# Kernel optimization log

Measured on AMD Instinct MI355X. Metric: run time of the kernel, lower is better.

## Reference

```python
import jax, jax.numpy as jnp
import numpy as np

EMBED_DIM = 512
NUM_HEADS = 8
HEAD_DIM = EMBED_DIM // NUM_HEADS


def setup_inputs() -> dict:
    key = jax.random.key(0)
    ks = jax.random.split(key, 9)
    C = EMBED_DIM
    s = 1.0 / np.sqrt(C)
    x = jax.random.normal(ks[0], (1, 4096, C), dtype=jnp.float32)
    Wq = jax.random.uniform(ks[1], (C, C), jnp.float32, -s, s)
    bq = jax.random.uniform(ks[2], (C,), jnp.float32, -s, s)
    Wk = jax.random.uniform(ks[3], (C, C), jnp.float32, -s, s)
    bk = jax.random.uniform(ks[4], (C,), jnp.float32, -s, s)
    Wv = jax.random.uniform(ks[5], (C, C), jnp.float32, -s, s)
    bv = jax.random.uniform(ks[6], (C,), jnp.float32, -s, s)
    Wo = jax.random.uniform(ks[7], (C, C), jnp.float32, -s, s)
    bo = jax.random.uniform(ks[8], (C,), jnp.float32, -s, s)
    return {"x": x, "Wq": Wq, "bq": bq, "Wk": Wk, "bk": bk,
            "Wv": Wv, "bv": bv, "Wo": Wo, "bo": bo}


def reference(x, Wq, bq, Wk, bk, Wv, bv, Wo, bo):
    B, N, C = x.shape
    H, D = NUM_HEADS, HEAD_DIM
    # QKV projections, split into heads: [B, H, N, D]
    def proj(W, b):
        y = x @ W + b
        return y.reshape(B, N, H, D).transpose(0, 2, 1, 3)
    Q, K, V = proj(Wq, bq), proj(Wk, bk), proj(Wv, bv)
    # NOTE: original scales by 1/sqrt(embed_dim), NOT 1/sqrt(head_dim)
    scale = 1.0 / jnp.sqrt(jnp.float32(C)).astype(x.dtype)
    scores = jnp.einsum('bhnd,bhmd->bhnm', Q, K) * scale  # [B,H,N,N]
    attn = jax.nn.softmax(scores, axis=-1)
    out = jnp.einsum('bhnm,bhmd->bhnd', attn, V)  # [B,H,N,D]
    out = out.transpose(0, 2, 1, 3).reshape(B, N, C)
    return out @ Wo + bo
```

## Files before the change

kernel.cpp:

```cpp
#include <hip/hip_runtime.h>
#include <hip/hip_bf16.h>

#define SEQ 4096
#define CDIM 512
#define NHEAD 8
#define HDIM 64
#define KVB 64
#define NSPLIT 4
#define TILES_PER_SPLIT (SEQ / KVB / NSPLIT)

typedef __attribute__((ext_vector_type(8))) short bf16x8;
typedef __attribute__((ext_vector_type(4))) float f32x4;
typedef __attribute__((ext_vector_type(16))) float f32x16;

__device__ __forceinline__ short f2b(float f) {
  union { float f; unsigned u; } v; v.f = f;
  unsigned u = v.u;
  unsigned r = u + 0x7fffu + ((u >> 16) & 1u);
  return (short)(r >> 16);
}
__device__ __forceinline__ float b2f(short s) {
  union { unsigned u; float f; } v; v.u = ((unsigned)(unsigned short)s) << 16;
  return v.f;
}
__device__ __forceinline__ unsigned pk2(float a, float b) {
  union { __hip_bfloat162 h; unsigned u; } z;
  z.h = __float22bfloat162_rn(make_float2(a, b));
  return z.u;
}

__global__ __launch_bounds__(256) void prep_kernel(
    const float* __restrict__ x,
    const float* __restrict__ Wq, const float* __restrict__ Wk,
    const float* __restrict__ Wv, const float* __restrict__ Wo,
    short* __restrict__ xb,
    short* __restrict__ Wqt, short* __restrict__ Wkt,
    short* __restrict__ Wvt, short* __restrict__ Wot) {
  __shared__ short tile[32][33];
  int b = blockIdx.x, tid = threadIdx.x;
  if (b < 2048) {
    int i = (b * 256 + tid) * 4;
    float4 v = *(const float4*)(x + i);
    short4 o;
    o.x = f2b(v.x); o.y = f2b(v.y); o.z = f2b(v.z); o.w = f2b(v.w);
    *(short4*)(xb + i) = o;
    return;
  }
  int t = b - 2048;
  int mat = t >> 8; t &= 255;
  const float* W = mat == 0 ? Wq : mat == 1 ? Wk : mat == 2 ? Wv : Wo;
  short* Wt = mat == 0 ? Wqt : mat == 1 ? Wkt : mat == 2 ? Wvt : Wot;
  int n0 = (t & 15) * 32, k0 = (t >> 4) * 32;
  int tx = tid & 31, ty = tid >> 5;
  for (int i = 0; i < 32; i += 8)
    tile[ty + i][tx] = f2b(W[(size_t)(k0 + ty + i) * CDIM + n0 + tx]);
  __syncthreads();
  for (int i = 0; i < 32; i += 8)
    Wt[(size_t)(n0 + ty + i) * CDIM + k0 + tx] = tile[tx][ty + i];
}

__global__ __launch_bounds__(256) void qkv_gemm_kernel(
    const short* __restrict__ A,
    const short* __restrict__ Wqt, const short* __restrict__ Wkt, const short* __restrict__ Wvt,
    const float* __restrict__ bq, const float* __restrict__ bk, const float* __restrict__ bv,
    short* __restrict__ Qb, short* __restrict__ Kb, short* __restrict__ Vtb) {
  __shared__ short As[64 * 64];
  __shared__ short Bs[64 * 64];
  const int z = blockIdx.z;
  const short* Bt = z == 0 ? Wqt : z == 1 ? Wkt : Wvt;
  const float* bias = z == 0 ? bq : z == 1 ? bk : bv;
  const int m0 = blockIdx.x * 64, n0 = blockIdx.y * 64;
  const int tid = threadIdx.x;
  const int w = tid >> 6, lane = tid & 63, g = lane >> 4, l16 = lane & 15;
  f32x4 acc[4] = {};
  for (int kt = 0; kt < CDIM; kt += 64) {
    __syncthreads();
    for (int it = 0; it < 2; ++it) {
      int c = tid + it * 256;
      int r = c >> 3, cc = (c & 7) * 8;
      int sw = r * 64 + (cc ^ ((r & 7) * 8));
      *(bf16x8*)(As + sw) = *(const bf16x8*)(A + (size_t)(m0 + r) * CDIM + kt + cc);
      *(bf16x8*)(Bs + sw) = *(const bf16x8*)(Bt + (size_t)(n0 + r) * CDIM + kt + cc);
    }
    __syncthreads();
    const int ar = w * 16 + l16;
    for (int ks = 0; ks < 2; ++ks) {
      int c0 = ks * 32 + 8 * g;
      bf16x8 af = *(const bf16x8*)(As + ar * 64 + (c0 ^ ((ar & 7) * 8)));
      for (int ni = 0; ni < 4; ++ni) {
        int br = ni * 16 + l16;
        bf16x8 bf = *(const bf16x8*)(Bs + br * 64 + (c0 ^ ((br & 7) * 8)));
        acc[ni] = __builtin_amdgcn_mfma_f32_16x16x32_bf16(af, bf, acc[ni], 0, 0, 0);
      }
    }
  }
  for (int ni = 0; ni < 4; ++ni) {
    int col = n0 + ni * 16 + l16;
    float bv_ = bias[col];
    for (int j = 0; j < 4; ++j) {
      int row = m0 + w * 16 + g * 4 + j;
      float v = acc[ni][j] + bv_;
      if (z == 0)      Qb[(size_t)row * CDIM + col] = f2b(v);
      else if (z == 1) Kb[(size_t)row * CDIM + col] = f2b(v);
      else             Vtb[(size_t)col * SEQ + row] = f2b(v);
    }
  }
}

__global__ __launch_bounds__(256) void out_gemm_kernel(
    const short* __restrict__ A, const short* __restrict__ Bt,
    const float* __restrict__ bias, float* __restrict__ out) {
  __shared__ short As[64 * 64];
  __shared__ short Bs[64 * 64];
  const int m0 = blockIdx.x * 64, n0 = blockIdx.y * 64;
  const int tid = threadIdx.x;
  const int w = tid >> 6, lane = tid & 63, g = lane >> 4, l16 = lane & 15;
  f32x4 acc[4] = {};
  for (int kt = 0; kt < CDIM; kt += 64) {
    __syncthreads();
    for (int it = 0; it < 2; ++it) {
      int c = tid + it * 256;
      int r = c >> 3, cc = (c & 7) * 8;
      int sw = r * 64 + (cc ^ ((r & 7) * 8));
      *(bf16x8*)(As + sw) = *(const bf16x8*)(A + (size_t)(m0 + r) * CDIM + kt + cc);
      *(bf16x8*)(Bs + sw) = *(const bf16x8*)(Bt + (size_t)(n0 + r) * CDIM + kt + cc);
    }
    __syncthreads();
    const int ar = w * 16 + l16;
    for (int ks = 0; ks < 2; ++ks) {
      int c0 = ks * 32 + 8 * g;
      bf16x8 af = *(const bf16x8*)(As + ar * 64 + (c0 ^ ((ar & 7) * 8)));
      for (int ni = 0; ni < 4; ++ni) {
        int br = ni * 16 + l16;
        bf16x8 bf = *(const bf16x8*)(Bs + br * 64 + (c0 ^ ((br & 7) * 8)));
        acc[ni] = __builtin_amdgcn_mfma_f32_16x16x32_bf16(af, bf, acc[ni], 0, 0, 0);
      }
    }
  }
  for (int ni = 0; ni < 4; ++ni) {
    int col = n0 + ni * 16 + l16;
    float bv_ = bias[col];
    for (int j = 0; j < 4; ++j) {
      int row = m0 + w * 16 + g * 4 + j;
      out[(size_t)row * CDIM + col] = acc[ni][j] + bv_;
    }
  }
}

__global__ __launch_bounds__(512, 4) void attn_kernel(
    const short* __restrict__ Qb,
    const short* __restrict__ Kb,
    const short* __restrict__ Vtb,
    short* __restrict__ Op0, short* __restrict__ Op1,
    short* __restrict__ Op2, short* __restrict__ Op3,
    float* __restrict__ lpart) {
  __shared__ __align__(16) char arena[49152];
  __shared__ float lzp[4][32];
  short* KsB = (short*)arena;
  short* VsB = (short*)(arena + 24576);
  const int bid = blockIdx.x;
  const int h = bid & 7;
  const int rest = bid >> 3;
  const int split = rest & 3;
  const int q0 = (rest >> 2) * 128;
  const int kvbase = split * (TILES_PER_SPLIT * KVB);
  const int tid = threadIdx.x;
  const int wid = tid >> 6, lane = tid & 63;
  const int l31 = lane & 31, hi = lane >> 5;
  const int rh = wid >> 1, kq = wid & 1;
  const float scale2 = 0.06375872274f;

  short* Opart = split == 0 ? Op0 : split == 1 ? Op1 : split == 2 ? Op2 : Op3;

  bf16x8 qf[4];
  {
    int qrow = q0 + rh * 32 + l31;
#pragma unroll
    for (int kst = 0; kst < 4; ++kst) {
      bf16x8 q = *(const bf16x8*)(Qb + (size_t)qrow * CDIM + h * 64 + kst * 16 + hi * 8);
#pragma unroll
      for (int i = 0; i < 8; ++i) q[i] = f2b(b2f(q[i]) * scale2);
      qf[kst] = q;
    }
  }

  const int srow = tid >> 3;
  const int scol8 = 8 * ((tid & 7) ^ (srow & 7));
  const short* kstage = Kb + (size_t)(kvbase + srow) * CDIM + h * 64 + scol8;
  const short* vstage = Vtb + (size_t)(h * 64 + srow) * SEQ + kvbase + scol8;
  auto stage = [&](short* sK, short* sV) {
    __builtin_amdgcn_global_load_lds(
        (const __attribute__((address_space(1))) void*)kstage,
        (__attribute__((address_space(3))) void*)(sK + tid * 8), 16, 0, 0);
    __builtin_amdgcn_global_load_lds(
        (const __attribute__((address_space(1))) void*)vstage,
        (__attribute__((address_space(3))) void*)(sV + tid * 8), 16, 0, 0);
    kstage += KVB * CDIM;
    vstage += KVB;
  };

  f32x16 osum[2] = {};
  float lsum = 0.f;
  unsigned w[8];

  auto softmax = [&](f32x16& s) {
    float ls0 = 0.f, ls1 = 0.f;
#pragma unroll
    for (int m = 0; m < 8; ++m) {
      float p0 = __builtin_amdgcn_exp2f(s[2 * m]);
      float p1 = __builtin_amdgcn_exp2f(s[2 * m + 1]);
      ls0 += p0; ls1 += p1;
      w[m] = pk2(p0, p1);
    }
    lsum += ls0 + ls1;
  };

  auto phase = [&](const short* vbuf, const short* kbuf, short* sK, short* sV, bool do_st) {
    if (do_st) stage(sK, sV);
    union { unsigned u[4]; bf16x8 v; } pf0, pf1;
#if __has_builtin(__builtin_amdgcn_permlane32_swap)
    {
      auto a0 = __builtin_amdgcn_permlane32_swap(w[0], w[2], false, false);
      auto a1 = __builtin_amdgcn_permlane32_swap(w[1], w[3], false, false);
      auto a2 = __builtin_amdgcn_permlane32_swap(w[4], w[6], false, false);
      auto a3 = __builtin_amdgcn_permlane32_swap(w[5], w[7], false, false);
      pf0.u[0] = a0[0]; pf0.u[1] = a1[0]; pf0.u[2] = a0[1]; pf0.u[3] = a1[1];
      pf1.u[0] = a2[0]; pf1.u[1] = a3[0]; pf1.u[2] = a2[1]; pf1.u[3] = a3[1];
    }
#else
    {
      unsigned t0 = hi ? w[0] : w[2], t1 = hi ? w[1] : w[3];
      unsigned t2 = hi ? w[4] : w[6], t3 = hi ? w[5] : w[7];
      unsigned r0 = __shfl_xor(t0, 32), r1 = __shfl_xor(t1, 32);
      unsigned r2 = __shfl_xor(t2, 32), r3 = __shfl_xor(t3, 32);
      pf0.u[0] = hi ? r0 : w[0]; pf0.u[1] = hi ? r1 : w[1];
      pf0.u[2] = hi ? w[2] : r0; pf0.u[3] = hi ? w[3] : r1;
      pf1.u[0] = hi ? r2 : w[4]; pf1.u[1] = hi ? r3 : w[5];
      pf1.u[2] = hi ? w[6] : r2; pf1.u[3] = hi ? w[7] : r3;
    }
#endif
    f32x16 s = {};
    __builtin_amdgcn_s_setprio(1);
#pragma unroll
    for (int kst = 0; kst < 4; ++kst) {
      int row = kq * 32 + l31;
      bf16x8 kf = *(const bf16x8*)(kbuf + row * 64 + ((kst * 16 + hi * 8) ^ ((row & 7) * 8)));
      s = __builtin_amdgcn_mfma_f32_32x32x16_bf16(kf, qf[kst], s, 0, 0, 0);
    }
#pragma unroll
    for (int dm = 0; dm < 2; ++dm) {
      int vrow = dm * 32 + l31;
      bf16x8 vf0 = *(const bf16x8*)(vbuf + vrow * 64 + ((kq * 32 + hi * 8) ^ ((vrow & 7) * 8)));
      osum[dm] = __builtin_amdgcn_mfma_f32_32x32x16_bf16(vf0, pf0.v, osum[dm], 0, 0, 0);
      bf16x8 vf1 = *(const bf16x8*)(vbuf + vrow * 64 + ((kq * 32 + 16 + hi * 8) ^ ((vrow & 7) * 8)));
      osum[dm] = __builtin_amdgcn_mfma_f32_32x32x16_bf16(vf1, pf1.v, osum[dm], 0, 0, 0);
    }
    __builtin_amdgcn_s_setprio(0);
    softmax(s);
    __syncthreads();
  };

  stage(KsB, VsB);
  __syncthreads();
  stage(KsB + 4096, VsB + 4096);
  {
    f32x16 s = {};
#pragma unroll
    for (int kst = 0; kst < 4; ++kst) {
      int row = kq * 32 + l31;
      bf16x8 kf = *(const bf16x8*)(KsB + row * 64 + ((kst * 16 + hi * 8) ^ ((row & 7) * 8)));
      s = __builtin_amdgcn_mfma_f32_32x32x16_bf16(kf, qf[kst], s, 0, 0, 0);
    }
    softmax(s);
  }
  __syncthreads();

  for (int t = 0; t < TILES_PER_SPLIT - 1; t += 3) {
    phase(VsB,        KsB + 4096, KsB + 8192, VsB + 8192, t + 2 < TILES_PER_SPLIT);
    phase(VsB + 4096, KsB + 8192, KsB,        VsB,        t + 3 < TILES_PER_SPLIT);
    phase(VsB + 8192, KsB,        KsB + 4096, VsB + 4096, t + 4 < TILES_PER_SPLIT);
  }

  {
    union { unsigned u[4]; bf16x8 v; } pf0, pf1;
#if __has_builtin(__builtin_amdgcn_permlane32_swap)
    auto a0 = __builtin_amdgcn_permlane32_swap(w[0], w[2], false, false);
    auto a1 = __builtin_amdgcn_permlane32_swap(w[1], w[3], false, false);
    auto a2 = __builtin_amdgcn_permlane32_swap(w[4], w[6], false, false);
    auto a3 = __builtin_amdgcn_permlane32_swap(w[5], w[7], false, false);
    pf0.u[0] = a0[0]; pf0.u[1] = a1[0]; pf0.u[2] = a0[1]; pf0.u[3] = a1[1];
    pf1.u[0] = a2[0]; pf1.u[1] = a3[0]; pf1.u[2] = a2[1]; pf1.u[3] = a3[1];
#else
    unsigned t0 = hi ? w[0] : w[2], t1 = hi ? w[1] : w[3];
    unsigned t2 = hi ? w[4] : w[6], t3 = hi ? w[5] : w[7];
    unsigned r0 = __shfl_xor(t0, 32), r1 = __shfl_xor(t1, 32);
    unsigned r2 = __shfl_xor(t2, 32), r3 = __shfl_xor(t3, 32);
    pf0.u[0] = hi ? r0 : w[0]; pf0.u[1] = hi ? r1 : w[1];
    pf0.u[2] = hi ? w[2] : r0; pf0.u[3] = hi ? w[3] : r1;
    pf1.u[0] = hi ? r2 : w[4]; pf1.u[1] = hi ? r3 : w[5];
    pf1.u[2] = hi ? w[6] : r2; pf1.u[3] = hi ? w[7] : r3;
#endif
#pragma unroll
    for (int dm = 0; dm < 2; ++dm) {
      int vrow = dm * 32 + l31;
      bf16x8 vf0 = *(const bf16x8*)(VsB + vrow * 64 + ((kq * 32 + hi * 8) ^ ((vrow & 7) * 8)));
      osum[dm] = __builtin_amdgcn_mfma_f32_32x32x16_bf16(vf0, pf0.v, osum[dm], 0, 0, 0);
      bf16x8 vf1 = *(const bf16x8*)(VsB + vrow * 64 + ((kq * 32 + 16 + hi * 8) ^ ((vrow & 7) * 8)));
      osum[dm] = __builtin_amdgcn_mfma_f32_32x32x16_bf16(vf1, pf1.v, osum[dm], 0, 0, 0);
    }
  }

  lsum += __shfl_xor(lsum, 32);

  __syncthreads();
  float* bufA = (float*)arena;
#define OD(dm, r) ((dm) * 32 + ((r) & 3) + 8 * ((r) >> 2) + 4 * hi)
#define OADDR(dm, r) (rh * 2112 + OD(dm, r) * 33 + l31)
  if (kq == 1) {
    if (hi == 0) lzp[rh][l31] = lsum;
#pragma unroll
    for (int dm = 0; dm < 2; ++dm)
#pragma unroll
      for (int r = 0; r < 16; ++r) bufA[OADDR(dm, r)] = osum[dm][r];
  }
  __syncthreads();
  if (kq == 0) {
#pragma unroll
    for (int dm = 0; dm < 2; ++dm)
#pragma unroll
      for (int r = 0; r < 16; ++r) {
        float v = osum[dm][r] + bufA[OADDR(dm, r)];
        bufA[OADDR(dm, r)] = v;
      }
    float lt = lsum + lzp[rh][l31];
    if (hi == 0)
      lpart[(size_t)(split * NHEAD + h) * SEQ + q0 + rh * 32 + l31] = lt;
  }
  __syncthreads();
#undef OD
#undef OADDR

  {
    int q_ = tid >> 2;
    int dc = (tid & 3) * 16;
    int qr = q_ >> 5, ql = q_ & 31;
    short ov[16];
#pragma unroll
    for (int i = 0; i < 16; ++i)
      ov[i] = f2b(bufA[qr * 2112 + (dc + i) * 33 + ql]);
    *(bf16x8*)(Opart + (size_t)(q0 + q_) * CDIM + h * 64 + dc) = *(bf16x8*)(ov);
    *(bf16x8*)(Opart + (size_t)(q0 + q_) * CDIM + h * 64 + dc + 8) = *(bf16x8*)(ov + 8);
  }
}

__global__ __launch_bounds__(256) void combine_kernel(
    const short* __restrict__ p0, const short* __restrict__ p1,
    const short* __restrict__ p2, const short* __restrict__ p3,
    const float* __restrict__ lpart, short* __restrict__ Ab) {
  int t = blockIdx.x * 256 + threadIdx.x;
  size_t base = (size_t)t * 8;
  int q = (int)(base >> 9), c = (int)(base & 511), h = c >> 6;
  float l = lpart[(size_t)(0 * NHEAD + h) * SEQ + q] +
            lpart[(size_t)(1 * NHEAD + h) * SEQ + q] +
            lpart[(size_t)(2 * NHEAD + h) * SEQ + q] +
            lpart[(size_t)(3 * NHEAD + h) * SEQ + q];
  float rinv = 1.f / l;
  bf16x8 a0 = *(const bf16x8*)(p0 + base);
  bf16x8 a1 = *(const bf16x8*)(p1 + base);
  bf16x8 a2 = *(const bf16x8*)(p2 + base);
  bf16x8 a3 = *(const bf16x8*)(p3 + base);
  short ov[8];
#pragma unroll
  for (int i = 0; i < 8; ++i)
    ov[i] = f2b((b2f(a0[i]) + b2f(a1[i]) + b2f(a2[i]) + b2f(a3[i])) * rinv);
  *(bf16x8*)(Ab + base) = *(bf16x8*)(ov);
}

extern "C" void kernel_launch(void* const* d_in, const int* in_sizes, int n_in,
                              void* d_out, int out_size, void* d_ws, size_t ws_size,
                              hipStream_t stream) {
  const float* x  = (const float*)d_in[0];
  const float* Wq = (const float*)d_in[1];
  const float* bq = (const float*)d_in[2];
  const float* Wk = (const float*)d_in[3];
  const float* bk = (const float*)d_in[4];
  const float* Wv = (const float*)d_in[5];
  const float* bv = (const float*)d_in[6];
  const float* Wo = (const float*)d_in[7];
  const float* bo = (const float*)d_in[8];
  float* out = (float*)d_out;

  short* ws = (short*)d_ws;
  size_t off = 0;
  short* xb  = ws + off; off += (size_t)SEQ * CDIM;
  short* Wqt = ws + off; off += (size_t)CDIM * CDIM;
  short* Wkt = ws + off; off += (size_t)CDIM * CDIM;
  short* Wvt = ws + off; off += (size_t)CDIM * CDIM;
  short* Wot = ws + off; off += (size_t)CDIM * CDIM;
  short* Qb  = ws + off; off += (size_t)SEQ * CDIM;
  short* Kb  = ws + off; off += (size_t)SEQ * CDIM;
  short* Vtb = ws + off; off += (size_t)CDIM * SEQ;
  short* Ab  = ws + off; off += (size_t)SEQ * CDIM;
  short* Op1 = ws + off; off += (size_t)SEQ * CDIM;
  short* Op2 = ws + off; off += (size_t)SEQ * CDIM;
  short* Op3 = ws + off; off += (size_t)SEQ * CDIM;
  float* lpart = (float*)(ws + off); off += (size_t)NSPLIT * NHEAD * SEQ * 2;
  short* Op0 = xb;

  prep_kernel<<<2048 + 4 * 256, 256, 0, stream>>>(x, Wq, Wk, Wv, Wo, xb, Wqt, Wkt, Wvt, Wot);
  qkv_gemm_kernel<<<dim3(SEQ / 64, CDIM / 64, 3), 256, 0, stream>>>(
      xb, Wqt, Wkt, Wvt, bq, bk, bv, Qb, Kb, Vtb);
  attn_kernel<<<(SEQ / 128) * NHEAD * NSPLIT, 512, 0, stream>>>(
      Qb, Kb, Vtb, Op0, Op1, Op2, Op3, lpart);
  combine_kernel<<<SEQ * CDIM / 8 / 256, 256, 0, stream>>>(Op0, Op1, Op2, Op3, lpart, Ab);
  out_gemm_kernel<<<dim3(SEQ / 64, CDIM / 64), 256, 0, stream>>>(Ab, Wot, bo, out);
}
```

Measured before the change: 87.46 us.

## Rewrite projection GEMMs with 128x64 tiles, 32x32 MFMA and direct global-to-LDS loads

Replaces the 64x64-tile QKV and output projection GEMMs with a shared 128x64-tile core in which each wave computes a 64x32 block using 32x32x16 bf16 MFMA. Operand tiles are loaded straight into LDS with global_load_lds, keeping the XOR swizzle on the source address. The aim is more reuse per loaded tile, fewer LDS fragment reads per MFMA and fewer register round trips when staging. The trade-offs are half as many blocks in the grid and the same scattered scalar epilogue stores, including the strided transposed V writes.

```diff
diff --git a/kernel.cpp b/kernel.cpp
--- a/kernel.cpp
+++ b/kernel.cpp
@@ -59,92 +59,93 @@
     Wt[(size_t)(n0 + ty + i) * CDIM + k0 + tx] = tile[tx][ty + i];
 }
 
-__global__ __launch_bounds__(256) void qkv_gemm_kernel(
+#define GEMM128_CORE(Asrc, Btsrc)                                                          \
+  f32x16 acc[2] = {};                                                                      \
+  const int tid = threadIdx.x;                                                             \
+  const int wid = tid >> 6, lane = tid & 63, l31 = lane & 31, hi = lane >> 5;              \
+  const int wr = wid >> 1, wc = wid & 1;                                                   \
+  for (int kt = 0; kt < CDIM; kt += 64) {                                                  \
+    __syncthreads();                                                                       \
+    _Pragma("unroll")                                                                      \
+    for (int i = 0; i < 4; ++i) {                                                          \
+      int idx = i * 256 + tid, row = idx >> 3, seg = idx & 7;                              \
+      int sc = (seg ^ (row & 7)) * 8;                                                      \
+      __builtin_amdgcn_global_load_lds(                                                    \
+          (const __attribute__((address_space(1))) void*)(Asrc + (size_t)(m0 + row) * CDIM + kt + sc), \
+          (__attribute__((address_space(3))) void*)(As + idx * 8), 16, 0, 0);              \
+    }                                                                                      \
+    _Pragma("unroll")                                                                      \
+    for (int i = 0; i < 2; ++i) {                                                          \
+      int idx = i * 256 + tid, row = idx >> 3, seg = idx & 7;                              \
+      int sc = (seg ^ (row & 7)) * 8;                                                      \
+      __builtin_amdgcn_global_load_lds(                                                    \
+          (const __attribute__((address_space(1))) void*)(Btsrc + (size_t)(n0 + row) * CDIM + kt + sc), \
+          (__attribute__((address_space(3))) void*)(Bs + idx * 8), 16, 0, 0);              \
+    }                                                                                      \
+    __syncthreads();                                                                       \
+    _Pragma("unroll")                                                                      \
+    for (int ks = 0; ks < 4; ++ks) {                                                       \
+      int brow = wc * 32 + l31;                                                            \
+      bf16x8 bfr = *(const bf16x8*)(Bs + brow * 64 + ((ks * 16 + hi * 8) ^ ((brow & 7) * 8))); \
+      _Pragma("unroll")                                                                    \
+      for (int ai = 0; ai < 2; ++ai) {                                                     \
+        int arow = wr * 64 + ai * 32 + l31;                                                \
+        bf16x8 afr = *(const bf16x8*)(As + arow * 64 + ((ks * 16 + hi * 8) ^ ((arow & 7) * 8))); \
+        acc[ai] = __builtin_amdgcn_mfma_f32_32x32x16_bf16(afr, bfr, acc[ai], 0, 0, 0);     \
+      }                                                                                    \
+    }                                                                                      \
+  }
+
+__global__ __launch_bounds__(256) void qkv128_kernel(
     const short* __restrict__ A,
     const short* __restrict__ Wqt, const short* __restrict__ Wkt, const short* __restrict__ Wvt,
     const float* __restrict__ bq, const float* __restrict__ bk, const float* __restrict__ bv,
     short* __restrict__ Qb, short* __restrict__ Kb, short* __restrict__ Vtb) {
-  __shared__ short As[64 * 64];
-  __shared__ short Bs[64 * 64];
+  __shared__ __align__(16) short As[128 * 64];
+  __shared__ __align__(16) short Bs[64 * 64];
   const int z = blockIdx.z;
   const short* Bt = z == 0 ? Wqt : z == 1 ? Wkt : Wvt;
   const float* bias = z == 0 ? bq : z == 1 ? bk : bv;
-  const int m0 = blockIdx.x * 64, n0 = blockIdx.y * 64;
-  const int tid = threadIdx.x;
-  const int w = tid >> 6, lane = tid & 63, g = lane >> 4, l16 = lane & 15;
-  f32x4 acc[4] = {};
-  for (int kt = 0; kt < CDIM; kt += 64) {
-    __syncthreads();
-    for (int it = 0; it < 2; ++it) {
-      int c = tid + it * 256;
-      int r = c >> 3, cc = (c & 7) * 8;
-      int sw = r * 64 + (cc ^ ((r & 7) * 8));
-      *(bf16x8*)(As + sw) = *(const bf16x8*)(A + (size_t)(m0 + r) * CDIM + kt + cc);
-      *(bf16x8*)(Bs + sw) = *(const bf16x8*)(Bt + (size_t)(n0 + r) * CDIM + kt + cc);
-    }
-    __syncthreads();
-    const int ar = w * 16 + l16;
-    for (int ks = 0; ks < 2; ++ks) {
-      int c0 = ks * 32 + 8 * g;
-      bf16x8 af = *(const bf16x8*)(As + ar * 64 + (c0 ^ ((ar & 7) * 8)));
-      for (int ni = 0; ni < 4; ++ni) {
-        int br = ni * 16 + l16;
-        bf16x8 bf = *(const bf16x8*)(Bs + br * 64 + (c0 ^ ((br & 7) * 8)));
-        acc[ni] = __builtin_amdgcn_mfma_f32_16x16x32_bf16(af, bf, acc[ni], 0, 0, 0);
+  const int m0 = blockIdx.x * 128, n0 = blockIdx.y * 64;
+  GEMM128_CORE(A, Bt)
+  const int ncol = n0 + wc * 32 + l31;
+  const float bn = bias[ncol];
+  if (z != 2) {
+    short* D = z == 0 ? Qb : Kb;
+#pragma unroll
+    for (int ai = 0; ai < 2; ++ai)
+#pragma unroll
+      for (int r = 0; r < 16; ++r) {
+        int m = m0 + wr * 64 + ai * 32 + (r & 3) + 8 * (r >> 2) + 4 * hi;
+        D[(size_t)m * CDIM + ncol] = f2b(acc[ai][r] + bn);
       }
-    }
-  }
-  for (int ni = 0; ni < 4; ++ni) {
-    int col = n0 + ni * 16 + l16;
-    float bv_ = bias[col];
-    for (int j = 0; j < 4; ++j) {
-      int row = m0 + w * 16 + g * 4 + j;
-      float v = acc[ni][j] + bv_;
-      if (z == 0)      Qb[(size_t)row * CDIM + col] = f2b(v);
-      else if (z == 1) Kb[(size_t)row * CDIM + col] = f2b(v);
-      else             Vtb[(size_t)col * SEQ + row] = f2b(v);
-    }
-  }
-}
-
-__global__ __launch_bounds__(256) void out_gemm_kernel(
+  } else {
+#pragma unroll
+    for (int ai = 0; ai < 2; ++ai)
+#pragma unroll
+      for (int r = 0; r < 16; ++r) {
+        int m = m0 + wr * 64 + ai * 32 + (r & 3) + 8 * (r >> 2) + 4 * hi;
+        Vtb[(size_t)ncol * SEQ + m] = f2b(acc[ai][r] + bn);
+      }
+  }
+}
+
+__global__ __launch_bounds__(256) void out128_kernel(
     const short* __restrict__ A, const short* __restrict__ Bt,
     const float* __restrict__ bias, float* __restrict__ out) {
-  __shared__ short As[64 * 64];
-  __shared__ short Bs[64 * 64];
-  const int m0 = blockIdx.x * 64, n0 = blockIdx.y * 64;
-  const int tid = threadIdx.x;
-  const int w = tid >> 6, lane = tid & 63, g = lane >> 4, l16 = lane & 15;
-  f32x4 acc[4] = {};
-  for (int kt = 0; kt < CDIM; kt += 64) {
-    __syncthreads();
-    for (int it = 0; it < 2; ++it) {
-      int c = tid + it * 256;
-      int r = c >> 3, cc = (c & 7) * 8;
-      int sw = r * 64 + (cc ^ ((r & 7) * 8));
-      *(bf16x8*)(As + sw) = *(const bf16x8*)(A + (size_t)(m0 + r) * CDIM + kt + cc);
-      *(bf16x8*)(Bs + sw) = *(const bf16x8*)(Bt + (size_t)(n0 + r) * CDIM + kt + cc);
-    }
-    __syncthreads();
-    const int ar = w * 16 + l16;
-    for (int ks = 0; ks < 2; ++ks) {
-      int c0 = ks * 32 + 8 * g;
-      bf16x8 af = *(const bf16x8*)(As + ar * 64 + (c0 ^ ((ar & 7) * 8)));
-      for (int ni = 0; ni < 4; ++ni) {
-        int br = ni * 16 + l16;
-        bf16x8 bf = *(const bf16x8*)(Bs + br * 64 + (c0 ^ ((br & 7) * 8)));
-        acc[ni] = __builtin_amdgcn_mfma_f32_16x16x32_bf16(af, bf, acc[ni], 0, 0, 0);
-      }
-    }
-  }
-  for (int ni = 0; ni < 4; ++ni) {
-    int col = n0 + ni * 16 + l16;
-    float bv_ = bias[col];
-    for (int j = 0; j < 4; ++j) {
-      int row = m0 + w * 16 + g * 4 + j;
-      out[(size_t)row * CDIM + col] = acc[ni][j] + bv_;
-    }
-  }
+  __shared__ __align__(16) short As[128 * 64];
+  __shared__ __align__(16) short Bs[64 * 64];
+  const int m0 = blockIdx.x * 128, n0 = blockIdx.y * 64;
+  GEMM128_CORE(A, Bt)
+  const int ncol = n0 + wc * 32 + l31;
+  const float bn = bias[ncol];
+#pragma unroll
+  for (int ai = 0; ai < 2; ++ai)
+#pragma unroll
+    for (int r = 0; r < 16; ++r) {
+      int m = m0 + wr * 64 + ai * 32 + (r & 3) + 8 * (r >> 2) + 4 * hi;
+      out[(size_t)m * CDIM + ncol] = acc[ai][r] + bn;
+    }
 }
 
 __global__ __launch_bounds__(512, 4) void attn_kernel(
@@ -408,10 +409,10 @@
   short* Op0 = xb;
 
   prep_kernel<<<2048 + 4 * 256, 256, 0, stream>>>(x, Wq, Wk, Wv, Wo, xb, Wqt, Wkt, Wvt, Wot);
-  qkv_gemm_kernel<<<dim3(SEQ / 64, CDIM / 64, 3), 256, 0, stream>>>(
+  qkv128_kernel<<<dim3(SEQ / 128, CDIM / 64, 3), 256, 0, stream>>>(
       xb, Wqt, Wkt, Wvt, bq, bk, bv, Qb, Kb, Vtb);
   attn_kernel<<<(SEQ / 128) * NHEAD * NSPLIT, 512, 0, stream>>>(
       Qb, Kb, Vtb, Op0, Op1, Op2, Op3, lpart);
   combine_kernel<<<SEQ * CDIM / 8 / 256, 256, 0, stream>>>(Op0, Op1, Op2, Op3, lpart, Ab);
-  out_gemm_kernel<<<dim3(SEQ / 64, CDIM / 64), 256, 0, stream>>>(Ab, Wot, bo, out);
-}
+  out128_kernel<<<dim3(SEQ / 128, CDIM / 64), 256, 0, stream>>>(Ab, Wot, bo, out);
+}
```

Result: faster. 81.77 us (-6.5%).
